# Kernel optimization log

Measured on AMD Instinct MI355X. Metric: run time of the kernel, lower is better.

## Reference

```python
import jax, jax.numpy as jnp
import numpy as np

B, C, H, W, P = 16, 5, 256, 256, 8
SF, ED, HS, NH, FF = 64, 128, 512, 4, 2048
L, NE, NS, NC, TK = 4, 6, 2, 2, 2
EPS = 1e-5


def _layernorm(x, g, b):
    m = x.mean(-1, keepdims=True)
    v = ((x - m) ** 2).mean(-1, keepdims=True)
    return (x - m) * jax.lax.rsqrt(v + EPS) * g + b


def setup_inputs() -> dict:
    key = jax.random.key(0)
    ks = iter(jax.random.split(key, 64))

    def rn(shape, s=0.02):
        return jax.random.normal(next(ks), shape, jnp.float32) * s

    return {
        "x": jax.random.normal(next(ks), (B, C, H, W), jnp.float32),
        "tok_w1": rn((SF, C * P * P)), "tok_b1": jnp.zeros((SF,), jnp.float32),
        "tok_w2": rn((ED, SF)), "tok_b2": jnp.zeros((ED,), jnp.float32),
        "proj_w": rn((HS, ED)), "proj_b": jnp.zeros((HS,), jnp.float32),
        "attn_wqkv": rn((L, 3 * HS, HS)), "attn_bqkv": jnp.zeros((L, 3 * HS), jnp.float32),
        "attn_wo": rn((L, HS, HS)), "attn_bo": jnp.zeros((L, HS), jnp.float32),
        "ln1_g": jnp.ones((L, HS), jnp.float32), "ln1_b": jnp.zeros((L, HS), jnp.float32),
        "spec_router_w": rn((L, NE, HS)),
        "spec_fc1_w": rn((L, NE, FF, HS)), "spec_fc1_b": jnp.zeros((L, NE, FF), jnp.float32),
        "spec_fc2_w": rn((L, NE, HS, FF)), "spec_fc2_b": jnp.zeros((L, NE, HS), jnp.float32),
        "shr_router_w": rn((L, NS, HS)),
        "shr_fc1_w": rn((L, NS, FF, HS)), "shr_fc1_b": jnp.zeros((L, NS, FF), jnp.float32),
        "shr_fc2_w": rn((L, NS, HS, FF)), "shr_fc2_b": jnp.zeros((L, NS, HS), jnp.float32),
        "lnm_g": jnp.ones((L, HS), jnp.float32), "lnm_b": jnp.zeros((L, HS), jnp.float32),
        "ln2_g": jnp.ones((L, HS), jnp.float32), "ln2_b": jnp.zeros((L, HS), jnp.float32),
        "cls_w": rn((NC, HS)), "cls_b": jnp.zeros((NC,), jnp.float32),
    }


def reference(x, tok_w1, tok_b1, tok_w2, tok_b2, proj_w, proj_b,
              attn_wqkv, attn_bqkv, attn_wo, attn_bo, ln1_g, ln1_b,
              spec_router_w, spec_fc1_w, spec_fc1_b, spec_fc2_w, spec_fc2_b,
              shr_router_w, shr_fc1_w, shr_fc1_b, shr_fc2_w, shr_fc2_b,
              lnm_g, lnm_b, ln2_g, ln2_b, cls_w, cls_b):
    b = x.shape[0]
    nH, nW = H // P, W // P
    S = nH * nW
    # PatchTokeniser: [B,C,H,W] -> [B, nP, C*p*p] (patch-major, channel inside)
    t = x.reshape(b, C, nH, P, nW, P).transpose(0, 2, 4, 1, 3, 5).reshape(b, S, C * P * P)
    z = jax.nn.relu(t @ tok_w1.T + tok_b1)
    z = jax.nn.relu(z @ tok_w2.T + tok_b2)  # [B,S,ED]
    # sinusoidal positional encoding (dropout is identity at inference)
    pos = np.arange(S, dtype=np.float32)[:, None]
    div = np.exp(np.arange(0, ED, 2, dtype=np.float32) * (-np.log(10000.0) / ED))
    pe = np.zeros((S, ED), np.float32)
    pe[:, 0::2] = np.sin(pos * div)
    pe[:, 1::2] = np.cos(pos * div)
    z = z + jnp.asarray(pe)
    h = z @ proj_w.T + proj_b  # [B,S,HS]
    hd = HS // NH
    scale = 1.0 / np.sqrt(hd).astype(np.float32)
    for l in range(L):
        # --- self attention (torch MHA, batch_first, eval mode) ---
        qkv = h @ attn_wqkv[l].T + attn_bqkv[l]
        q, k, v = jnp.split(qkv, 3, axis=-1)
        q = q.reshape(b, S, NH, hd).transpose(0, 2, 1, 3)
        k = k.reshape(b, S, NH, hd).transpose(0, 2, 1, 3)
        v = v.reshape(b, S, NH, hd).transpose(0, 2, 1, 3)
        att = jax.nn.softmax(jnp.einsum('bhqd,bhkd->bhqk', q, k) * scale, axis=-1)
        a = jnp.einsum('bhqk,bhkd->bhqd', att, v).transpose(0, 2, 1, 3).reshape(b, S, HS)
        a = a @ attn_wo[l].T + attn_bo[l]
        h = _layernorm(h + a, ln1_g[l], ln1_b[l])
        # --- SpecificMoE: top-k routing; combine weights replace dense masking ---
        probs = jax.nn.softmax(h @ spec_router_w[l].T, axis=-1)  # [B,S,NE]
        topk_p, topk_i = jax.lax.top_k(probs, TK)
        topk_p = topk_p / (topk_p.sum(-1, keepdims=True) + 1e-9)
        comb = (jax.nn.one_hot(topk_i, NE, dtype=h.dtype) * topk_p[..., None]).sum(-2)  # [B,S,NE]
        spec = jnp.zeros_like(h)
        for e in range(NE):
            hid = jax.nn.gelu(h @ spec_fc1_w[l, e].T + spec_fc1_b[l, e], approximate=False)
            spec = spec + comb[..., e:e + 1] * (hid @ spec_fc2_w[l, e].T + spec_fc2_b[l, e])
        # --- SharedMoE: softmax-weighted sum of all shared experts ---
        sp = jax.nn.softmax(h @ shr_router_w[l].T, axis=-1)  # [B,S,NS]
        shar = jnp.zeros_like(h)
        for e in range(NS):
            hid = jax.nn.gelu(h @ shr_fc1_w[l, e].T + shr_fc1_b[l, e], approximate=False)
            shar = shar + sp[..., e:e + 1] * (hid @ shr_fc2_w[l, e].T + shr_fc2_b[l, e])
        m = _layernorm(h + spec + shar, lnm_g[l], lnm_b[l])
        h = _layernorm(h + m, ln2_g[l], ln2_b[l])
    pooled = h.mean(axis=1)  # [B,HS]
    return pooled @ cls_w.T + cls_b  # [B,NC]
```

## Files before the change

kernel.cpp:

```cpp
#include <hip/hip_runtime.h>

typedef unsigned short u16;
using bf16x8 = __attribute__((ext_vector_type(8))) short;
using f32x4  = __attribute__((ext_vector_type(4))) float;

__device__ __forceinline__ float bf2f(u16 u) {
  union { unsigned int i; float f; } v; v.i = ((unsigned int)u) << 16; return v.f;
}
__device__ __forceinline__ u16 f2bf(float f) {
  union { float f; unsigned int i; } v; v.f = f;
  unsigned int r = v.i + 0x7fffu + ((v.i >> 16) & 1u);
  return (u16)(r >> 16);
}

__device__ __forceinline__ void async_copy16(const u16* g, u16* l) {
  __builtin_amdgcn_global_load_lds(
      (const __attribute__((address_space(1))) void*)g,
      (__attribute__((address_space(3))) void*)l, 16, 0, 0);
}

template<int ACT, int OUTMODE, int HAS_BIAS>
__global__ __launch_bounds__(256)
void gemm_tile(const u16* __restrict__ A, const u16* __restrict__ B,
               void* __restrict__ C,
               const float* __restrict__ bias,
               const float* __restrict__ rowscale, int rs_stride,
               int lda, int ldb, int ldc, int K, int inner,
               long long sAo, long long sAi, long long sBo, long long sBi,
               long long sCo, long long sCi)
{
  __shared__ u16 Als[128 * 32];
  __shared__ u16 Bls[128 * 32];

  const int tid  = threadIdx.x;
  const int lane = tid & 63;
  const int wave = tid >> 6;

  const int z  = blockIdx.z;
  const int zo = z / inner;
  const int zi = z - zo * inner;

  const u16* Ab = A + zo * sAo + zi * sAi;
  const u16* Bb = B + zo * sBo + zi * sBi;

  const long long n0 = (long long)blockIdx.x * 128;
  const long long m0 = (long long)blockIdx.y * 128;

  const int c0 = tid, c1 = tid + 256;
  const int rA0 = c0 >> 2, kA0 = (c0 & 3) * 8;
  const int rA1 = c1 >> 2, kA1 = (c1 & 3) * 8;

  const u16* gA0 = Ab + (n0 + rA0) * lda + kA0;
  const u16* gA1 = Ab + (n0 + rA1) * lda + kA1;
  const u16* gB0 = Bb + (m0 + rA0) * ldb + kA0;
  const u16* gB1 = Bb + (m0 + rA1) * ldb + kA1;

  const int fr = lane & 15;
  const int fq = lane >> 4;
  const u16* Ard = &Als[(((wave >> 1) * 64) + fr) * 32 + fq * 8];
  const u16* Brd = &Bls[(((wave & 1) * 64) + fr) * 32 + fq * 8];

  f32x4 acc[4][4] = {};

  for (int kt = 0; kt < K; kt += 32) {
    async_copy16(gA0, &Als[c0 * 8]);
    async_copy16(gA1, &Als[c1 * 8]);
    async_copy16(gB0, &Bls[c0 * 8]);
    async_copy16(gB1, &Bls[c1 * 8]);
    gA0 += 32; gA1 += 32; gB0 += 32; gB1 += 32;
    __syncthreads();

    bf16x8 af[4], bfv[4];
#pragma unroll
    for (int i = 0; i < 4; ++i) af[i]  = *(const bf16x8*)(Ard + i * (16 * 32));
#pragma unroll
    for (int j = 0; j < 4; ++j) bfv[j] = *(const bf16x8*)(Brd + j * (16 * 32));
#pragma unroll
    for (int i = 0; i < 4; ++i)
#pragma unroll
      for (int j = 0; j < 4; ++j)
        acc[i][j] = __builtin_amdgcn_mfma_f32_16x16x32_bf16(af[i], bfv[j], acc[i][j], 0, 0, 0);
    __syncthreads();
  }

  const long long cb = zo * sCo + zi * sCi;
  const int wr = (wave >> 1) * 64;
  const int wc = (wave & 1) * 64;
#pragma unroll
  for (int i = 0; i < 4; ++i) {
#pragma unroll
    for (int r = 0; r < 4; ++r) {
      const long long row = n0 + wr + i * 16 + fq * 4 + r;
      float rs = 0.f;
      if (OUTMODE == 2) rs = rowscale[row * (long long)rs_stride];
#pragma unroll
      for (int j = 0; j < 4; ++j) {
        const long long col = m0 + wc + j * 16 + fr;
        float v = acc[i][j][r];
        if (HAS_BIAS) v += bias[col];
        if (ACT == 1) v = fmaxf(v, 0.f);
        if (ACT == 2) v = 0.5f * v * (1.f + erff(v * 0.70710678118654752f));
        const long long idx = cb + row * ldc + col;
        if (OUTMODE == 0)      ((float*)C)[idx] = v;
        else if (OUTMODE == 1) ((u16*)C)[idx] = f2bf(v);
        else                   ((float*)C)[idx] += rs * v;
      }
    }
  }
}

template<int ACT, int OUT, int BIAS>
static inline void run_gemm(hipStream_t st,
    const u16* A, const u16* B, void* C, const float* bias,
    const float* rowscale, int rs_stride,
    int N, int M, int K, int lda, int ldb, int ldc,
    int batch, int inner,
    long long sAo, long long sAi, long long sBo, long long sBi,
    long long sCo, long long sCi)
{
  dim3 g(N / 128, M / 128, batch);
  gemm_tile<ACT, OUT, BIAS><<<g, dim3(256), 0, st>>>(
      A, B, C, bias, rowscale, rs_stride, lda, ldb, ldc, K, inner,
      sAo, sAi, sBo, sBi, sCo, sCi);
}

__global__ void cast_bf16_k(const float* __restrict__ s, u16* __restrict__ d, long long n)
{
  long long i = (long long)blockIdx.x * blockDim.x + threadIdx.x;
  const long long stride = (long long)gridDim.x * blockDim.x;
  for (; i < n; i += stride) d[i] = f2bf(s[i]);
}

__global__ void transpose_f32_k(const float* __restrict__ s, float* __restrict__ d,
                                int rows, int cols)
{
  int i = blockIdx.x * blockDim.x + threadIdx.x;
  if (i < rows * cols) { int r = i / cols, c = i - r * cols; d[c * rows + r] = s[i]; }
}

__global__ __launch_bounds__(64)
void tokenizer_k(const float* __restrict__ x, const float* __restrict__ w1T,
                 const float* __restrict__ b1, const float* __restrict__ w2T,
                 const float* __restrict__ b2, u16* __restrict__ z)
{
  const int token = blockIdx.x;
  const int b = token >> 10, s = token & 1023;
  const int ph = s >> 5, pw = s & 31;
  const int lane = threadIdx.x;
  __shared__ float t[320];
  __shared__ float z1[64];
  const int py = lane >> 3, px = lane & 7;
  const float* xp = x + (size_t)b * 5 * 65536 + (size_t)(ph * 8 + py) * 256 + pw * 8 + px;
#pragma unroll
  for (int c = 0; c < 5; ++c) t[c * 64 + lane] = xp[(size_t)c * 65536];
  __syncthreads();
  float acc = b1[lane];
  for (int k = 0; k < 320; ++k) acc = fmaf(t[k], w1T[k * 64 + lane], acc);
  z1[lane] = fmaxf(acc, 0.f);
  __syncthreads();
  float a0 = b2[lane], a1 = b2[lane + 64];
  for (int k = 0; k < 64; ++k) {
    const float zv = z1[k];
    a0 = fmaf(zv, w2T[k * 128 + lane], a0);
    a1 = fmaf(zv, w2T[k * 128 + lane + 64], a1);
  }
  a0 = fmaxf(a0, 0.f); a1 = fmaxf(a1, 0.f);
  const float fs = (float)s;
  const int d0 = lane, d1 = lane + 64;
  const float div0 = expf(-logf(10000.f) * (float)(d0 & ~1) / 128.f);
  const float div1 = expf(-logf(10000.f) * (float)(d1 & ~1) / 128.f);
  const float pe0 = (d0 & 1) ? cosf(fs * div0) : sinf(fs * div0);
  const float pe1 = (d1 & 1) ? cosf(fs * div1) : sinf(fs * div1);
  z[(size_t)token * 128 + d0] = f2bf(a0 + pe0);
  z[(size_t)token * 128 + d1] = f2bf(a1 + pe1);
}

__global__ void transpose_v_k(const u16* __restrict__ qkv, u16* __restrict__ vT)
{
  __shared__ u16 tile[32][33];
  const int z = blockIdx.z;
  const int b = z >> 2, hh = z & 3;
  const int s0 = blockIdx.x * 32, d0 = blockIdx.y * 32;
  const int tx = threadIdx.x;
  for (int i = threadIdx.y; i < 32; i += 8)
    tile[i][tx] = qkv[(long long)(b * 1024 + s0 + i) * 1536 + 1024 + hh * 128 + d0 + tx];
  __syncthreads();
  for (int j = threadIdx.y; j < 32; j += 8)
    vT[((long long)z * 128 + d0 + j) * 1024 + s0 + tx] = tile[tx][j];
}

__global__ __launch_bounds__(256)
void softmax_k(u16* __restrict__ P, float scale)
{
  const long long row = blockIdx.x;
  u16* p = P + row * 1024;
  const int tid = threadIdx.x;
  float v[4];
#pragma unroll
  for (int j = 0; j < 4; ++j) v[j] = bf2f(p[tid + j * 256]) * scale;
  __shared__ float red[256];
  float mx = fmaxf(fmaxf(v[0], v[1]), fmaxf(v[2], v[3]));
  red[tid] = mx; __syncthreads();
  for (int s = 128; s > 0; s >>= 1) { if (tid < s) red[tid] = fmaxf(red[tid], red[tid + s]); __syncthreads(); }
  mx = red[0]; __syncthreads();
  float sum = 0.f;
#pragma unroll
  for (int j = 0; j < 4; ++j) { v[j] = expf(v[j] - mx); sum += v[j]; }
  red[tid] = sum; __syncthreads();
  for (int s = 128; s > 0; s >>= 1) { if (tid < s) red[tid] += red[tid + s]; __syncthreads(); }
  const float inv = 1.f / red[0];
#pragma unroll
  for (int j = 0; j < 4; ++j) p[tid + j * 256] = f2bf(v[j] * inv);
}

__global__ __launch_bounds__(256)
void ln_add_k(float* __restrict__ h, const float* __restrict__ a,
              const float* __restrict__ g, const float* __restrict__ b,
              u16* __restrict__ hbf)
{
  const long long t = blockIdx.x;
  const int tid = threadIdx.x;
  float* hp = h + t * 512;
  const float* ap = a + t * 512;
  const float x0 = hp[tid] + ap[tid];
  const float x1 = hp[tid + 256] + ap[tid + 256];
  __shared__ float r1[256], r2[256];
  r1[tid] = x0 + x1; r2[tid] = x0 * x0 + x1 * x1;
  __syncthreads();
  for (int s = 128; s > 0; s >>= 1) { if (tid < s) { r1[tid] += r1[tid + s]; r2[tid] += r2[tid + s]; } __syncthreads(); }
  const float mean = r1[0] * (1.f / 512.f);
  const float var  = r2[0] * (1.f / 512.f) - mean * mean;
  const float rstd = rsqrtf(var + 1e-5f);
  const float y0 = (x0 - mean) * rstd * g[tid] + b[tid];
  const float y1 = (x1 - mean) * rstd * g[tid + 256] + b[tid + 256];
  hp[tid] = y0; hp[tid + 256] = y1;
  hbf[t * 512 + tid] = f2bf(y0); hbf[t * 512 + tid + 256] = f2bf(y1);
}

__global__ __launch_bounds__(256)
void merge_ln_k(float* __restrict__ h, const float* __restrict__ macc,
                const float* __restrict__ g1, const float* __restrict__ b1,
                const float* __restrict__ g2, const float* __restrict__ b2,
                u16* __restrict__ hbf)
{
  const long long t = blockIdx.x;
  const int tid = threadIdx.x;
  float* hp = h + t * 512;
  const float* mp = macc + t * 512;
  const float hx0 = hp[tid], hx1 = hp[tid + 256];
  const float s0 = hx0 + mp[tid], s1 = hx1 + mp[tid + 256];
  __shared__ float r1[256], r2[256];
  r1[tid] = s0 + s1; r2[tid] = s0 * s0 + s1 * s1;
  __syncthreads();
  for (int s = 128; s > 0; s >>= 1) { if (tid < s) { r1[tid] += r1[tid + s]; r2[tid] += r2[tid + s]; } __syncthreads(); }
  float mean = r1[0] * (1.f / 512.f);
  float var  = r2[0] * (1.f / 512.f) - mean * mean;
  float rstd = rsqrtf(var + 1e-5f);
  const float m0v = (s0 - mean) * rstd * g1[tid] + b1[tid];
  const float m1v = (s1 - mean) * rstd * g1[tid + 256] + b1[tid + 256];
  const float z0 = hx0 + m0v, z1 = hx1 + m1v;
  __syncthreads();
  r1[tid] = z0 + z1; r2[tid] = z0 * z0 + z1 * z1;
  __syncthreads();
  for (int s = 128; s > 0; s >>= 1) { if (tid < s) { r1[tid] += r1[tid + s]; r2[tid] += r2[tid + s]; } __syncthreads(); }
  mean = r1[0] * (1.f / 512.f);
  var  = r2[0] * (1.f / 512.f) - mean * mean;
  rstd = rsqrtf(var + 1e-5f);
  const float y0 = (z0 - mean) * rstd * g2[tid] + b2[tid];
  const float y1 = (z1 - mean) * rstd * g2[tid + 256] + b2[tid + 256];
  hp[tid] = y0; hp[tid + 256] = y1;
  hbf[t * 512 + tid] = f2bf(y0); hbf[t * 512 + tid + 256] = f2bf(y1);
}

__global__ __launch_bounds__(64)
void router_k(const float* __restrict__ h, const float* __restrict__ sw,
              const float* __restrict__ hw, float* __restrict__ comb,
              float* __restrict__ sp)
{
  const long long t = blockIdx.x;
  const int lane = threadIdx.x;
  const float* hp = h + t * 512;
  float v[8];
#pragma unroll
  for (int j = 0; j < 8; ++j) v[j] = hp[lane + j * 64];

  float lg[6];
#pragma unroll
  for (int e = 0; e < 6; ++e) {
    const float* w = sw + e * 512;
    float d = 0.f;
#pragma unroll
    for (int j = 0; j < 8; ++j) d += v[j] * w[lane + j * 64];
#pragma unroll
    for (int off = 32; off > 0; off >>= 1) d += __shfl_xor(d, off);
    lg[e] = d;
  }
  float mx = lg[0];
#pragma unroll
  for (int e = 1; e < 6; ++e) mx = fmaxf(mx, lg[e]);
  float pp[6]; float sum = 0.f;
#pragma unroll
  for (int e = 0; e < 6; ++e) { pp[e] = expf(lg[e] - mx); sum += pp[e]; }
  const float inv = 1.f / sum;
#pragma unroll
  for (int e = 0; e < 6; ++e) pp[e] *= inv;

  int i1 = 0; float p1 = pp[0];
#pragma unroll
  for (int e = 1; e < 6; ++e) if (pp[e] > p1) { p1 = pp[e]; i1 = e; }
  int i2 = -1; float p2 = -1.f;
#pragma unroll
  for (int e = 0; e < 6; ++e) if (e != i1 && pp[e] > p2) { p2 = pp[e]; i2 = e; }
  const float den = 1.f / (p1 + p2 + 1e-9f);
  if (lane == 0) {
#pragma unroll
    for (int e = 0; e < 6; ++e)
      comb[t * 6 + e] = (e == i1) ? p1 * den : ((e == i2) ? p2 * den : 0.f);
  }

  float l0 = 0.f, l1 = 0.f;
#pragma unroll
  for (int j = 0; j < 8; ++j) {
    l0 += v[j] * hw[lane + j * 64];
    l1 += v[j] * hw[512 + lane + j * 64];
  }
#pragma unroll
  for (int off = 32; off > 0; off >>= 1) { l0 += __shfl_xor(l0, off); l1 += __shfl_xor(l1, off); }
  const float m2 = fmaxf(l0, l1);
  const float e0 = expf(l0 - m2), e1 = expf(l1 - m2);
  const float si = 1.f / (e0 + e1);
  if (lane == 0) { sp[t * 2 + 0] = e0 * si; sp[t * 2 + 1] = e1 * si; }
}

__global__ __launch_bounds__(256)
void pool_cls_k(const float* __restrict__ h, const float* __restrict__ cw,
                const float* __restrict__ cb, float* __restrict__ out)
{
  const int b = blockIdx.x;
  const int tid = threadIdx.x;
  const float* hp = h + (size_t)b * 1024 * 512;
  float s0 = 0.f, s1 = 0.f;
  for (int s = 0; s < 1024; ++s) {
    s0 += hp[(size_t)s * 512 + tid];
    s1 += hp[(size_t)s * 512 + tid + 256];
  }
  __shared__ float pooled[512];
  pooled[tid] = s0 * (1.f / 1024.f); pooled[tid + 256] = s1 * (1.f / 1024.f);
  __syncthreads();
  __shared__ float red[256];
  for (int c = 0; c < 2; ++c) {
    const float d = pooled[tid] * cw[c * 512 + tid] + pooled[tid + 256] * cw[c * 512 + tid + 256];
    red[tid] = d; __syncthreads();
    for (int s = 128; s > 0; s >>= 1) { if (tid < s) red[tid] += red[tid + s]; __syncthreads(); }
    if (tid == 0) out[b * 2 + c] = red[0] + cb[c];
    __syncthreads();
  }
}

extern "C" void kernel_launch(void* const* d_in, const int* in_sizes, int n_in,
                              void* d_out, int out_size, void* d_ws, size_t ws_size,
                              hipStream_t stream)
{
  (void)in_sizes; (void)n_in; (void)out_size; (void)ws_size;
  const float* x      = (const float*)d_in[0];
  const float* tok_w1 = (const float*)d_in[1];
  const float* tok_b1 = (const float*)d_in[2];
  const float* tok_w2 = (const float*)d_in[3];
  const float* tok_b2 = (const float*)d_in[4];
  const float* proj_w = (const float*)d_in[5];
  const float* proj_b = (const float*)d_in[6];
  const float* wqkv   = (const float*)d_in[7];
  const float* bqkv   = (const float*)d_in[8];
  const float* wo     = (const float*)d_in[9];
  const float* bo     = (const float*)d_in[10];
  const float* ln1_g  = (const float*)d_in[11];
  const float* ln1_b  = (const float*)d_in[12];
  const float* srw    = (const float*)d_in[13];
  const float* sfc1w  = (const float*)d_in[14];
  const float* sfc1b  = (const float*)d_in[15];
  const float* sfc2w  = (const float*)d_in[16];
  const float* sfc2b  = (const float*)d_in[17];
  const float* hrw    = (const float*)d_in[18];
  const float* hfc1w  = (const float*)d_in[19];
  const float* hfc1b  = (const float*)d_in[20];
  const float* hfc2w  = (const float*)d_in[21];
  const float* hfc2b  = (const float*)d_in[22];
  const float* lnm_g  = (const float*)d_in[23];
  const float* lnm_b  = (const float*)d_in[24];
  const float* ln2_g  = (const float*)d_in[25];
  const float* ln2_b  = (const float*)d_in[26];
  const float* cls_w  = (const float*)d_in[27];
  const float* cls_b  = (const float*)d_in[28];

  char* ws = (char*)d_ws;
  size_t off = 0;
  auto alloc = [&](size_t bytes) -> char* {
    char* p = ws + off;
    off = (off + bytes + 255) & ~(size_t)255;
    return p;
  };

  u16* proj_bf = (u16*)alloc((size_t)512 * 128 * 2);
  u16* qkvw_bf = (u16*)alloc((size_t)4 * 1536 * 512 * 2);
  u16* wow_bf  = (u16*)alloc((size_t)4 * 512 * 512 * 2);
  u16* sfc1_bf = (u16*)alloc((size_t)4 * 6 * 2048 * 512 * 2);
  u16* sfc2_bf = (u16*)alloc((size_t)4 * 6 * 512 * 2048 * 2);
  u16* hfc1_bf = (u16*)alloc((size_t)4 * 2 * 2048 * 512 * 2);
  u16* hfc2_bf = (u16*)alloc((size_t)4 * 2 * 512 * 2048 * 2);
  float* w1T   = (float*)alloc((size_t)320 * 64 * 4);
  float* w2T   = (float*)alloc((size_t)64 * 128 * 4);
  u16* zbf     = (u16*)alloc((size_t)16384 * 128 * 2);
  float* h     = (float*)alloc((size_t)16384 * 512 * 4);
  u16* hbf     = (u16*)alloc((size_t)16384 * 512 * 2);
  u16* vT      = (u16*)alloc((size_t)64 * 128 * 1024 * 2);
  u16* abf     = (u16*)alloc((size_t)16384 * 512 * 2);
  char* regA   = alloc((size_t)32 * 1024 * 1024 * 2);
  char* regB   = alloc((size_t)16384 * 1536 * 2);
  u16*   scores = (u16*)regA;
  float* af32   = (float*)regA;
  u16*   hid    = (u16*)regA;
  u16*   qkv    = (u16*)regB;
  float* macc   = (float*)regB;
  float* comb   = (float*)(regB + (size_t)16384 * 512 * 4);
  float* sp     = (float*)(regB + (size_t)16384 * 512 * 4 + (size_t)16384 * 6 * 4);

  cast_bf16_k<<<4096, 256, 0, stream>>>(proj_w, proj_bf, 65536LL);
  cast_bf16_k<<<4096, 256, 0, stream>>>(wqkv,   qkvw_bf, 3145728LL);
  cast_bf16_k<<<4096, 256, 0, stream>>>(wo,     wow_bf,  1048576LL);
  cast_bf16_k<<<4096, 256, 0, stream>>>(sfc1w,  sfc1_bf, 25165824LL);
  cast_bf16_k<<<4096, 256, 0, stream>>>(sfc2w,  sfc2_bf, 25165824LL);
  cast_bf16_k<<<4096, 256, 0, stream>>>(hfc1w,  hfc1_bf, 8388608LL);
  cast_bf16_k<<<4096, 256, 0, stream>>>(hfc2w,  hfc2_bf, 8388608LL);
  transpose_f32_k<<<(20480 + 255) / 256, 256, 0, stream>>>(tok_w1, w1T, 64, 320);
  transpose_f32_k<<<(8192 + 255) / 256, 256, 0, stream>>>(tok_w2, w2T, 128, 64);

  tokenizer_k<<<16384, 64, 0, stream>>>(x, w1T, tok_b1, w2T, tok_b2, zbf);
  run_gemm<0, 0, 1>(stream, zbf, proj_bf, h, proj_b, nullptr, 0,
                    16384, 512, 128, 128, 128, 512, 1, 1, 0, 0, 0, 0, 0, 0);
  cast_bf16_k<<<4096, 256, 0, stream>>>(h, hbf, 8388608LL);

  for (int l = 0; l < 4; ++l) {
    run_gemm<0, 1, 1>(stream, hbf, qkvw_bf + (size_t)l * 1536 * 512, qkv,
                      bqkv + l * 1536, nullptr, 0,
                      16384, 1536, 512, 512, 512, 1536, 1, 1, 0, 0, 0, 0, 0, 0);
    transpose_v_k<<<dim3(32, 4, 64), dim3(32, 8), 0, stream>>>(qkv, vT);
    for (int c = 0; c < 2; ++c) {
      const u16* qb = qkv + (size_t)c * 8 * 1024 * 1536;
      run_gemm<0, 1, 0>(stream, qb, qb + 512, scores, nullptr, nullptr, 0,
                        1024, 1024, 128, 1536, 1536, 1024, 32, 4,
                        1024LL * 1536, 128, 1024LL * 1536, 128,
                        4LL * 1024 * 1024, 1024LL * 1024);
      softmax_k<<<32768, 256, 0, stream>>>(scores, 0.08838834764831845f);
      run_gemm<0, 1, 0>(stream, scores, vT + (size_t)c * 8 * 4 * 128 * 1024,
                        abf + (size_t)c * 8 * 1024 * 512, nullptr, nullptr, 0,
                        1024, 128, 1024, 1024, 1024, 512, 32, 4,
                        4LL * 1024 * 1024, 1024LL * 1024,
                        4LL * 128 * 1024, 128LL * 1024,
                        1024LL * 512, 128);
    }
    run_gemm<0, 0, 1>(stream, abf, wow_bf + (size_t)l * 512 * 512, af32,
                      bo + l * 512, nullptr, 0,
                      16384, 512, 512, 512, 512, 512, 1, 1, 0, 0, 0, 0, 0, 0);
    hipMemsetAsync(macc, 0, (size_t)16384 * 512 * 4, stream);
    ln_add_k<<<16384, 256, 0, stream>>>(h, af32, ln1_g + l * 512, ln1_b + l * 512, hbf);
    router_k<<<16384, 64, 0, stream>>>(h, srw + (size_t)l * 6 * 512,
                                       hrw + (size_t)l * 2 * 512, comb, sp);
    for (int e = 0; e < 6; ++e) {
      const size_t wi = (size_t)(l * 6 + e);
      run_gemm<2, 1, 1>(stream, hbf, sfc1_bf + wi * 2048 * 512, hid,
                        sfc1b + wi * 2048, nullptr, 0,
                        16384, 2048, 512, 512, 512, 2048, 1, 1, 0, 0, 0, 0, 0, 0);
      run_gemm<0, 2, 1>(stream, hid, sfc2_bf + wi * 512 * 2048, macc,
                        sfc2b + wi * 512, comb + e, 6,
                        16384, 512, 2048, 2048, 2048, 512, 1, 1, 0, 0, 0, 0, 0, 0);
    }
    for (int e = 0; e < 2; ++e) {
      const size_t wi = (size_t)(l * 2 + e);
      run_gemm<2, 1, 1>(stream, hbf, hfc1_bf + wi * 2048 * 512, hid,
                        hfc1b + wi * 2048, nullptr, 0,
                        16384, 2048, 512, 512, 512, 2048, 1, 1, 0, 0, 0, 0, 0, 0);
      run_gemm<0, 2, 1>(stream, hid, hfc2_bf + wi * 512 * 2048, macc,
                        hfc2b + wi * 512, sp + e, 2,
                        16384, 512, 2048, 2048, 2048, 512, 1, 1, 0, 0, 0, 0, 0, 0);
    }
    merge_ln_k<<<16384, 256, 0, stream>>>(h, macc, lnm_g + l * 512, lnm_b + l * 512,
                                          ln2_g + l * 512, ln2_b + l * 512, hbf);
  }

  pool_cls_k<<<16, 256, 0, stream>>>(h, cls_w, cls_b, (float*)d_out);
}
```

Before: 6.571 ms.

## Run routed experts only on tokens selected by top-k gating

Builds per-expert token index lists from the combine weights, then runs the expert FC1 GEMM on gathered rows and the FC2 GEMM with split-K and atomic scatter-add back to token rows. Row blocks beyond the expert's token count exit early, avoiding dense computation for the roughly two-thirds of tokens each expert does not serve. Adds a list-building kernel, atomic accumulation with nondeterministic summation order, and gathered loads.

```diff
diff --git a/kernel.cpp b/kernel.cpp
--- a/kernel.cpp
+++ b/kernel.cpp
@@ -19,12 +19,14 @@
       (__attribute__((address_space(3))) void*)l, 16, 0, 0);
 }
 
-template<int ACT, int OUTMODE, int HAS_BIAS>
+template<int ACT, int OUTMODE, int HAS_BIAS, int GA>
 __global__ __launch_bounds__(256)
 void gemm_tile(const u16* __restrict__ A, const u16* __restrict__ B,
                void* __restrict__ C,
                const float* __restrict__ bias,
                const float* __restrict__ rowscale, int rs_stride,
+               const int* __restrict__ gidx, const int* __restrict__ gcnt,
+               int bias_zi0,
                int lda, int ldb, int ldc, int K, int inner,
                long long sAo, long long sAi, long long sBo, long long sBi,
                long long sCo, long long sCi)
@@ -40,18 +42,29 @@
   const int zo = z / inner;
   const int zi = z - zo * inner;
 
+  const long long n0 = (long long)blockIdx.x * 128;
+  const long long m0 = (long long)blockIdx.y * 128;
+
+  int cnt = 0x7fffffff;
+  if (GA || OUTMODE == 3) {
+    cnt = *gcnt;
+    if (n0 >= cnt) return;
+  }
+
   const u16* Ab = A + zo * sAo + zi * sAi;
   const u16* Bb = B + zo * sBo + zi * sBi;
-
-  const long long n0 = (long long)blockIdx.x * 128;
-  const long long m0 = (long long)blockIdx.y * 128;
 
   const int c0 = tid, c1 = tid + 256;
   const int rA0 = c0 >> 2, kA0 = (c0 & 3) * 8;
   const int rA1 = c1 >> 2, kA1 = (c1 & 3) * 8;
 
-  const u16* gA0 = Ab + (n0 + rA0) * lda + kA0;
-  const u16* gA1 = Ab + (n0 + rA1) * lda + kA1;
+  long long arow0 = n0 + rA0, arow1 = n0 + rA1;
+  if (GA) {
+    arow0 = (arow0 < cnt) ? (long long)gidx[arow0] : 0;
+    arow1 = (arow1 < cnt) ? (long long)gidx[arow1] : 0;
+  }
+  const u16* gA0 = Ab + arow0 * lda + kA0;
+  const u16* gA1 = Ab + arow1 * lda + kA1;
   const u16* gB0 = Bb + (m0 + rA0) * ldb + kA0;
   const u16* gB1 = Bb + (m0 + rA1) * ldb + kA1;
 
@@ -92,18 +105,27 @@
     for (int r = 0; r < 4; ++r) {
       const long long row = n0 + wr + i * 16 + fq * 4 + r;
       float rs = 0.f;
+      long long crow = row;
+      bool ok = true;
       if (OUTMODE == 2) rs = rowscale[row * (long long)rs_stride];
+      if (OUTMODE == 3) {
+        ok = row < cnt;
+        const int tok = ok ? gidx[row] : 0;
+        crow = tok;
+        rs = ok ? rowscale[(long long)tok * rs_stride] : 0.f;
+      }
 #pragma unroll
       for (int j = 0; j < 4; ++j) {
         const long long col = m0 + wc + j * 16 + fr;
         float v = acc[i][j][r];
-        if (HAS_BIAS) v += bias[col];
+        if (HAS_BIAS) { if (!bias_zi0 || zi == 0) v += bias[col]; }
         if (ACT == 1) v = fmaxf(v, 0.f);
         if (ACT == 2) v = 0.5f * v * (1.f + erff(v * 0.70710678118654752f));
-        const long long idx = cb + row * ldc + col;
+        const long long idx = cb + crow * ldc + col;
         if (OUTMODE == 0)      ((float*)C)[idx] = v;
         else if (OUTMODE == 1) ((u16*)C)[idx] = f2bf(v);
-        else                   ((float*)C)[idx] += rs * v;
+        else if (OUTMODE == 2) ((float*)C)[idx] += rs * v;
+        else if (ok)           atomicAdd(&((float*)C)[idx], rs * v);
       }
     }
   }
@@ -119,9 +141,9 @@
     long long sCo, long long sCi)
 {
   dim3 g(N / 128, M / 128, batch);
-  gemm_tile<ACT, OUT, BIAS><<<g, dim3(256), 0, st>>>(
-      A, B, C, bias, rowscale, rs_stride, lda, ldb, ldc, K, inner,
-      sAo, sAi, sBo, sBi, sCo, sCi);
+  gemm_tile<ACT, OUT, BIAS, 0><<<g, dim3(256), 0, st>>>(
+      A, B, C, bias, rowscale, rs_stride, nullptr, nullptr, 0,
+      lda, ldb, ldc, K, inner, sAo, sAi, sBo, sBi, sCo, sCi);
 }
 
 __global__ void cast_bf16_k(const float* __restrict__ s, u16* __restrict__ d, long long n)
@@ -330,6 +352,21 @@
   const float e0 = expf(l0 - m2), e1 = expf(l1 - m2);
   const float si = 1.f / (e0 + e1);
   if (lane == 0) { sp[t * 2 + 0] = e0 * si; sp[t * 2 + 1] = e1 * si; }
+}
+
+__global__ __launch_bounds__(256)
+void build_lists_k(const float* __restrict__ comb, int* __restrict__ cnt,
+                   int* __restrict__ idx)
+{
+  const int t = blockIdx.x * blockDim.x + threadIdx.x;
+  if (t >= 16384) return;
+#pragma unroll
+  for (int e = 0; e < 6; ++e) {
+    if (comb[(long long)t * 6 + e] > 0.f) {
+      const int pos = atomicAdd(&cnt[e], 1);
+      idx[e * 16384 + pos] = t;
+    }
+  }
 }
 
 __global__ __launch_bounds__(256)
@@ -414,6 +451,8 @@
   u16* hbf     = (u16*)alloc((size_t)16384 * 512 * 2);
   u16* vT      = (u16*)alloc((size_t)64 * 128 * 1024 * 2);
   u16* abf     = (u16*)alloc((size_t)16384 * 512 * 2);
+  int* cnt     = (int*)alloc((size_t)6 * 4);
+  int* idx     = (int*)alloc((size_t)6 * 16384 * 4);
   char* regA   = alloc((size_t)32 * 1024 * 1024 * 2);
   char* regB   = alloc((size_t)16384 * 1536 * 2);
   u16*   scores = (u16*)regA;
@@ -465,14 +504,18 @@
     ln_add_k<<<16384, 256, 0, stream>>>(h, af32, ln1_g + l * 512, ln1_b + l * 512, hbf);
     router_k<<<16384, 64, 0, stream>>>(h, srw + (size_t)l * 6 * 512,
                                        hrw + (size_t)l * 2 * 512, comb, sp);
+    hipMemsetAsync(cnt, 0, 6 * sizeof(int), stream);
+    build_lists_k<<<64, 256, 0, stream>>>(comb, cnt, idx);
     for (int e = 0; e < 6; ++e) {
       const size_t wi = (size_t)(l * 6 + e);
-      run_gemm<2, 1, 1>(stream, hbf, sfc1_bf + wi * 2048 * 512, hid,
-                        sfc1b + wi * 2048, nullptr, 0,
-                        16384, 2048, 512, 512, 512, 2048, 1, 1, 0, 0, 0, 0, 0, 0);
-      run_gemm<0, 2, 1>(stream, hid, sfc2_bf + wi * 512 * 2048, macc,
-                        sfc2b + wi * 512, comb + e, 6,
-                        16384, 512, 2048, 2048, 2048, 512, 1, 1, 0, 0, 0, 0, 0, 0);
+      gemm_tile<2, 1, 1, 1><<<dim3(128, 16, 1), dim3(256), 0, stream>>>(
+          hbf, sfc1_bf + wi * 2048 * 512, hid,
+          sfc1b + wi * 2048, nullptr, 0, idx + e * 16384, cnt + e, 0,
+          512, 512, 2048, 512, 1, 0, 0, 0, 0, 0, 0);
+      gemm_tile<0, 3, 1, 0><<<dim3(128, 4, 2), dim3(256), 0, stream>>>(
+          hid, sfc2_bf + wi * 512 * 2048, macc,
+          sfc2b + wi * 512, comb + e, 6, idx + e * 16384, cnt + e, 1,
+          2048, 2048, 512, 1024, 2, 0, 1024, 0, 1024, 0, 0);
     }
     for (int e = 0; e < 2; ++e) {
       const size_t wi = (size_t)(l * 2 + e);
```

After: 6.541 ms. No clear change (-0.5%).

## Route MoE tokens sparsely with grouped expert GEMMs and atomic scatter-add

Applied to the files above, without the earlier changes.

The specialist experts previously ran dense over all tokens and were masked by combine weights. Now the router builds per-expert token index lists, and grouped fc1/fc2 kernels process only the routed tokens (top-2 of 6, plus the shared experts) in FF chunks of 512. Results are scattered into the accumulator with float atomics. This removes the dense work on unselected experts, at the cost of gathered loads, atomic contention and nondeterministic summation order. The softmax kernel also switches to vectorized uint2 loads and stores.

```diff
diff --git a/kernel.cpp b/kernel.cpp
--- a/kernel.cpp
+++ b/kernel.cpp
@@ -1,6 +1,7 @@
 #include <hip/hip_runtime.h>
 
 typedef unsigned short u16;
+typedef unsigned int u32;
 using bf16x8 = __attribute__((ext_vector_type(8))) short;
 using f32x4  = __attribute__((ext_vector_type(4))) float;
 
@@ -19,12 +20,10 @@
       (__attribute__((address_space(3))) void*)l, 16, 0, 0);
 }
 
-template<int ACT, int OUTMODE, int HAS_BIAS>
+template<int OUTMODE, int HAS_BIAS>
 __global__ __launch_bounds__(256)
 void gemm_tile(const u16* __restrict__ A, const u16* __restrict__ B,
-               void* __restrict__ C,
-               const float* __restrict__ bias,
-               const float* __restrict__ rowscale, int rs_stride,
+               void* __restrict__ C, const float* __restrict__ bias,
                int lda, int ldb, int ldc, int K, int inner,
                long long sAo, long long sAi, long long sBo, long long sBi,
                long long sCo, long long sCi)
@@ -91,37 +90,200 @@
 #pragma unroll
     for (int r = 0; r < 4; ++r) {
       const long long row = n0 + wr + i * 16 + fq * 4 + r;
-      float rs = 0.f;
-      if (OUTMODE == 2) rs = rowscale[row * (long long)rs_stride];
 #pragma unroll
       for (int j = 0; j < 4; ++j) {
         const long long col = m0 + wc + j * 16 + fr;
         float v = acc[i][j][r];
         if (HAS_BIAS) v += bias[col];
-        if (ACT == 1) v = fmaxf(v, 0.f);
-        if (ACT == 2) v = 0.5f * v * (1.f + erff(v * 0.70710678118654752f));
         const long long idx = cb + row * ldc + col;
-        if (OUTMODE == 0)      ((float*)C)[idx] = v;
-        else if (OUTMODE == 1) ((u16*)C)[idx] = f2bf(v);
-        else                   ((float*)C)[idx] += rs * v;
+        if (OUTMODE == 0) ((float*)C)[idx] = v;
+        else              ((u16*)C)[idx] = f2bf(v);
       }
     }
   }
 }
 
-template<int ACT, int OUT, int BIAS>
+template<int OUT, int BIAS>
 static inline void run_gemm(hipStream_t st,
     const u16* A, const u16* B, void* C, const float* bias,
-    const float* rowscale, int rs_stride,
     int N, int M, int K, int lda, int ldb, int ldc,
     int batch, int inner,
     long long sAo, long long sAi, long long sBo, long long sBi,
     long long sCo, long long sCi)
 {
   dim3 g(N / 128, M / 128, batch);
-  gemm_tile<ACT, OUT, BIAS><<<g, dim3(256), 0, st>>>(
-      A, B, C, bias, rowscale, rs_stride, lda, ldb, ldc, K, inner,
-      sAo, sAi, sBo, sBi, sCo, sCi);
+  gemm_tile<OUT, BIAS><<<g, dim3(256), 0, st>>>(
+      A, B, C, bias, lda, ldb, ldc, K, inner, sAo, sAi, sBo, sBi, sCo, sCi);
+}
+
+__global__ __launch_bounds__(256)
+void moe_fc1_k(const u16* __restrict__ A, const u16* __restrict__ W,
+               const float* __restrict__ sb, const float* __restrict__ hb,
+               const int* __restrict__ idx, const int* __restrict__ cnt,
+               const int* __restrict__ poff,
+               u16* __restrict__ hid, int ff0)
+{
+  __shared__ u16 Als[128 * 32];
+  __shared__ u16 Bls[128 * 32];
+
+  const int tid  = threadIdx.x;
+  const int lane = tid & 63;
+  const int wave = tid >> 6;
+
+  const int row0 = blockIdx.x * 128;
+  if (row0 >= poff[8]) return;
+  int e = 0;
+  while (row0 >= poff[e + 1]) ++e;
+  const int r0 = row0 - poff[e];
+  const int ce = cnt[e];
+  if (r0 >= ce) return;
+  const int* gi = idx + e * 16384;
+
+  const int m0 = blockIdx.y * 128;
+  const u16* Wb = W + (size_t)e * 2048 * 512 + (size_t)(ff0 + m0) * 512;
+  const float* bias = (e < 6 ? sb + e * 2048 : hb + (e - 6) * 2048) + ff0;
+
+  const int c0 = tid, c1 = tid + 256;
+  const int rA0 = c0 >> 2, kA0 = (c0 & 3) * 8;
+  const int rA1 = c1 >> 2, kA1 = (c1 & 3) * 8;
+
+  const int t0 = (r0 + rA0 < ce) ? gi[r0 + rA0] : gi[r0];
+  const int t1 = (r0 + rA1 < ce) ? gi[r0 + rA1] : gi[r0];
+  const u16* gA0 = A + (size_t)t0 * 512 + kA0;
+  const u16* gA1 = A + (size_t)t1 * 512 + kA1;
+  const u16* gB0 = Wb + (size_t)rA0 * 512 + kA0;
+  const u16* gB1 = Wb + (size_t)rA1 * 512 + kA1;
+
+  const int fr = lane & 15;
+  const int fq = lane >> 4;
+  const u16* Ard = &Als[(((wave >> 1) * 64) + fr) * 32 + fq * 8];
+  const u16* Brd = &Bls[(((wave & 1) * 64) + fr) * 32 + fq * 8];
+
+  f32x4 acc[4][4] = {};
+
+  for (int kt = 0; kt < 512; kt += 32) {
+    async_copy16(gA0, &Als[c0 * 8]);
+    async_copy16(gA1, &Als[c1 * 8]);
+    async_copy16(gB0, &Bls[c0 * 8]);
+    async_copy16(gB1, &Bls[c1 * 8]);
+    gA0 += 32; gA1 += 32; gB0 += 32; gB1 += 32;
+    __syncthreads();
+
+    bf16x8 af[4], bfv[4];
+#pragma unroll
+    for (int i = 0; i < 4; ++i) af[i]  = *(const bf16x8*)(Ard + i * (16 * 32));
+#pragma unroll
+    for (int j = 0; j < 4; ++j) bfv[j] = *(const bf16x8*)(Brd + j * (16 * 32));
+#pragma unroll
+    for (int i = 0; i < 4; ++i)
+#pragma unroll
+      for (int j = 0; j < 4; ++j)
+        acc[i][j] = __builtin_amdgcn_mfma_f32_16x16x32_bf16(af[i], bfv[j], acc[i][j], 0, 0, 0);
+    __syncthreads();
+  }
+
+  const int wr = (wave >> 1) * 64;
+  const int wc = (wave & 1) * 64;
+#pragma unroll
+  for (int i = 0; i < 4; ++i) {
+#pragma unroll
+    for (int r = 0; r < 4; ++r) {
+      const long long row = row0 + wr + i * 16 + fq * 4 + r;
+#pragma unroll
+      for (int j = 0; j < 4; ++j) {
+        const int col = m0 + wc + j * 16 + fr;
+        float v = acc[i][j][r] + bias[col];
+        v = 0.5f * v * (1.f + erff(v * 0.70710678118654752f));
+        hid[row * 512 + col] = f2bf(v);
+      }
+    }
+  }
+}
+
+__global__ __launch_bounds__(256)
+void moe_fc2_k(const u16* __restrict__ hid, const u16* __restrict__ W,
+               const float* __restrict__ sb, const float* __restrict__ hb,
+               const float* __restrict__ comb, const float* __restrict__ sp,
+               const int* __restrict__ idx, const int* __restrict__ cnt,
+               const int* __restrict__ poff,
+               float* __restrict__ macc, int ff0)
+{
+  __shared__ u16 Als[128 * 32];
+  __shared__ u16 Bls[128 * 32];
+
+  const int tid  = threadIdx.x;
+  const int lane = tid & 63;
+  const int wave = tid >> 6;
+
+  const int row0 = blockIdx.x * 128;
+  if (row0 >= poff[8]) return;
+  int e = 0;
+  while (row0 >= poff[e + 1]) ++e;
+  const int r0 = row0 - poff[e];
+  const int ce = cnt[e];
+  if (r0 >= ce) return;
+  const int* gi = idx + e * 16384;
+
+  const int m0 = blockIdx.y * 128;
+  const u16* Wb = W + (size_t)e * 512 * 2048 + (size_t)m0 * 2048 + ff0;
+  const float* bias = (e < 6 ? sb + e * 512 : hb + (e - 6) * 512);
+
+  const int c0 = tid, c1 = tid + 256;
+  const int rA0 = c0 >> 2, kA0 = (c0 & 3) * 8;
+  const int rA1 = c1 >> 2, kA1 = (c1 & 3) * 8;
+
+  const u16* gA0 = hid + (size_t)(row0 + rA0) * 512 + kA0;
+  const u16* gA1 = hid + (size_t)(row0 + rA1) * 512 + kA1;
+  const u16* gB0 = Wb + (size_t)rA0 * 2048 + kA0;
+  const u16* gB1 = Wb + (size_t)rA1 * 2048 + kA1;
+
+  const int fr = lane & 15;
+  const int fq = lane >> 4;
+  const u16* Ard = &Als[(((wave >> 1) * 64) + fr) * 32 + fq * 8];
+  const u16* Brd = &Bls[(((wave & 1) * 64) + fr) * 32 + fq * 8];
+
+  f32x4 acc[4][4] = {};
+
+  for (int kt = 0; kt < 512; kt += 32) {
+    async_copy16(gA0, &Als[c0 * 8]);
+    async_copy16(gA1, &Als[c1 * 8]);
+    async_copy16(gB0, &Bls[c0 * 8]);
+    async_copy16(gB1, &Bls[c1 * 8]);
+    gA0 += 32; gA1 += 32; gB0 += 32; gB1 += 32;
+    __syncthreads();
+
+    bf16x8 af[4], bfv[4];
+#pragma unroll
+    for (int i = 0; i < 4; ++i) af[i]  = *(const bf16x8*)(Ard + i * (16 * 32));
+#pragma unroll
+    for (int j = 0; j < 4; ++j) bfv[j] = *(const bf16x8*)(Brd + j * (16 * 32));
+#pragma unroll
+    for (int i = 0; i < 4; ++i)
+#pragma unroll
+      for (int j = 0; j < 4; ++j)
+        acc[i][j] = __builtin_amdgcn_mfma_f32_16x16x32_bf16(af[i], bfv[j], acc[i][j], 0, 0, 0);
+    __syncthreads();
+  }
+
+  const int wr = (wave >> 1) * 64;
+  const int wc = (wave & 1) * 64;
+#pragma unroll
+  for (int i = 0; i < 4; ++i) {
+#pragma unroll
+    for (int r = 0; r < 4; ++r) {
+      const int lr = r0 + wr + i * 16 + fq * 4 + r;
+      if (lr >= ce) continue;
+      const int tok = gi[lr];
+      const float rs = (e < 6) ? comb[(size_t)tok * 6 + e] : sp[(size_t)tok * 2 + (e - 6)];
+#pragma unroll
+      for (int j = 0; j < 4; ++j) {
+        const int col = m0 + wc + j * 16 + fr;
+        float v = acc[i][j][r];
+        if (ff0 == 0) v += bias[col];
+        atomicAdd(&macc[(size_t)tok * 512 + col], rs * v);
+      }
+    }
+  }
 }
 
 __global__ void cast_bf16_k(const float* __restrict__ s, u16* __restrict__ d, long long n)
@@ -129,6 +291,24 @@
   long long i = (long long)blockIdx.x * blockDim.x + threadIdx.x;
   const long long stride = (long long)gridDim.x * blockDim.x;
   for (; i < n; i += stride) d[i] = f2bf(s[i]);
+}
+
+__global__ void cast_moe_w_k(const float* __restrict__ spec,
+                             const float* __restrict__ shr,
+                             u16* __restrict__ dst)
+{
+  long long i = (long long)blockIdx.x * blockDim.x + threadIdx.x;
+  const long long stride = (long long)gridDim.x * blockDim.x;
+  const long long n = 4LL * 8 * 1048576;
+  for (; i < n; i += stride) {
+    const long long l = i >> 23;
+    const long long r = i & ((1LL << 23) - 1);
+    const long long e = r >> 20;
+    const long long o = r & 1048575;
+    const float v = (e < 6) ? spec[(l * 6 + e) * 1048576 + o]
+                            : shr[(l * 2 + (e - 6)) * 1048576 + o];
+    dst[i] = f2bf(v);
+  }
 }
 
 __global__ void transpose_f32_k(const float* __restrict__ s, float* __restrict__ d,
@@ -193,11 +373,14 @@
 void softmax_k(u16* __restrict__ P, float scale)
 {
   const long long row = blockIdx.x;
-  u16* p = P + row * 1024;
+  uint2* p = (uint2*)(P + row * 1024);
   const int tid = threadIdx.x;
+  uint2 d = p[tid];
   float v[4];
-#pragma unroll
-  for (int j = 0; j < 4; ++j) v[j] = bf2f(p[tid + j * 256]) * scale;
+  v[0] = bf2f((u16)(d.x & 0xffff)) * scale;
+  v[1] = bf2f((u16)(d.x >> 16)) * scale;
+  v[2] = bf2f((u16)(d.y & 0xffff)) * scale;
+  v[3] = bf2f((u16)(d.y >> 16)) * scale;
   __shared__ float red[256];
   float mx = fmaxf(fmaxf(v[0], v[1]), fmaxf(v[2], v[3]));
   red[tid] = mx; __syncthreads();
@@ -209,8 +392,10 @@
   red[tid] = sum; __syncthreads();
   for (int s = 128; s > 0; s >>= 1) { if (tid < s) red[tid] += red[tid + s]; __syncthreads(); }
   const float inv = 1.f / red[0];
-#pragma unroll
-  for (int j = 0; j < 4; ++j) p[tid + j * 256] = f2bf(v[j] * inv);
+  uint2 o;
+  o.x = (u32)f2bf(v[0] * inv) | ((u32)f2bf(v[1] * inv) << 16);
+  o.y = (u32)f2bf(v[2] * inv) | ((u32)f2bf(v[3] * inv) << 16);
+  p[tid] = o;
 }
 
 __global__ __launch_bounds__(256)
@@ -275,7 +460,7 @@
 __global__ __launch_bounds__(64)
 void router_k(const float* __restrict__ h, const float* __restrict__ sw,
               const float* __restrict__ hw, float* __restrict__ comb,
-              float* __restrict__ sp)
+              float* __restrict__ sp, int* __restrict__ cnt, int* __restrict__ idx)
 {
   const long long t = blockIdx.x;
   const int lane = threadIdx.x;
@@ -316,6 +501,10 @@
 #pragma unroll
     for (int e = 0; e < 6; ++e)
       comb[t * 6 + e] = (e == i1) ? p1 * den : ((e == i2) ? p2 * den : 0.f);
+    int p = atomicAdd(&cnt[i1], 1); idx[i1 * 16384 + p] = (int)t;
+    p = atomicAdd(&cnt[i2], 1);     idx[i2 * 16384 + p] = (int)t;
+    idx[6 * 16384 + t] = (int)t;
+    idx[7 * 16384 + t] = (int)t;
   }
 
   float l0 = 0.f, l1 = 0.f;
@@ -330,6 +519,15 @@
   const float e0 = expf(l0 - m2), e1 = expf(l1 - m2);
   const float si = 1.f / (e0 + e1);
   if (lane == 0) { sp[t * 2 + 0] = e0 * si; sp[t * 2 + 1] = e1 * si; }
+}
+
+__global__ void offsets_k(int* __restrict__ cnt, int* __restrict__ poff)
+{
+  if (threadIdx.x == 0 && blockIdx.x == 0) {
+    cnt[6] = 16384; cnt[7] = 16384;
+    int o = 0; poff[0] = 0;
+    for (int e = 0; e < 8; ++e) { o += (cnt[e] + 127) & ~127; poff[e + 1] = o; }
+  }
 }
 
 __global__ __launch_bounds__(256)
@@ -361,7 +559,7 @@
                               void* d_out, int out_size, void* d_ws, size_t ws_size,
                               hipStream_t stream)
 {
-  (void)in_sizes; (void)n_in; (void)out_size; (void)ws_size;
+  (void)in_sizes; (void)n_in; (void)out_size;
   const float* x      = (const float*)d_in[0];
   const float* tok_w1 = (const float*)d_in[1];
   const float* tok_b1 = (const float*)d_in[2];
@@ -403,10 +601,8 @@
   u16* proj_bf = (u16*)alloc((size_t)512 * 128 * 2);
   u16* qkvw_bf = (u16*)alloc((size_t)4 * 1536 * 512 * 2);
   u16* wow_bf  = (u16*)alloc((size_t)4 * 512 * 512 * 2);
-  u16* sfc1_bf = (u16*)alloc((size_t)4 * 6 * 2048 * 512 * 2);
-  u16* sfc2_bf = (u16*)alloc((size_t)4 * 6 * 512 * 2048 * 2);
-  u16* hfc1_bf = (u16*)alloc((size_t)4 * 2 * 2048 * 512 * 2);
-  u16* hfc2_bf = (u16*)alloc((size_t)4 * 2 * 512 * 2048 * 2);
+  u16* w1comb  = (u16*)alloc((size_t)4 * 8 * 2048 * 512 * 2);
+  u16* w2comb  = (u16*)alloc((size_t)4 * 8 * 512 * 2048 * 2);
   float* w1T   = (float*)alloc((size_t)320 * 64 * 4);
   float* w2T   = (float*)alloc((size_t)64 * 128 * 4);
   u16* zbf     = (u16*)alloc((size_t)16384 * 128 * 2);
@@ -414,7 +610,10 @@
   u16* hbf     = (u16*)alloc((size_t)16384 * 512 * 2);
   u16* vT      = (u16*)alloc((size_t)64 * 128 * 1024 * 2);
   u16* abf     = (u16*)alloc((size_t)16384 * 512 * 2);
-  char* regA   = alloc((size_t)32 * 1024 * 1024 * 2);
+  int* cnt     = (int*)alloc((size_t)8 * 4);
+  int* poff    = (int*)alloc((size_t)9 * 4);
+  int* idx     = (int*)alloc((size_t)8 * 16384 * 4);
+  char* regA   = alloc((size_t)66560 * 512 * 2);
   char* regB   = alloc((size_t)16384 * 1536 * 2);
   u16*   scores = (u16*)regA;
   float* af32   = (float*)regA;
@@ -424,64 +623,58 @@
   float* comb   = (float*)(regB + (size_t)16384 * 512 * 4);
   float* sp     = (float*)(regB + (size_t)16384 * 512 * 4 + (size_t)16384 * 6 * 4);
 
+  if (off > ws_size) return;
+
   cast_bf16_k<<<4096, 256, 0, stream>>>(proj_w, proj_bf, 65536LL);
   cast_bf16_k<<<4096, 256, 0, stream>>>(wqkv,   qkvw_bf, 3145728LL);
   cast_bf16_k<<<4096, 256, 0, stream>>>(wo,     wow_bf,  1048576LL);
-  cast_bf16_k<<<4096, 256, 0, stream>>>(sfc1w,  sfc1_bf, 25165824LL);
-  cast_bf16_k<<<4096, 256, 0, stream>>>(sfc2w,  sfc2_bf, 25165824LL);
-  cast_bf16_k<<<4096, 256, 0, stream>>>(hfc1w,  hfc1_bf, 8388608LL);
-  cast_bf16_k<<<4096, 256, 0, stream>>>(hfc2w,  hfc2_bf, 8388608LL);
+  cast_moe_w_k<<<8192, 256, 0, stream>>>(sfc1w, hfc1w, w1comb);
+  cast_moe_w_k<<<8192, 256, 0, stream>>>(sfc2w, hfc2w, w2comb);
   transpose_f32_k<<<(20480 + 255) / 256, 256, 0, stream>>>(tok_w1, w1T, 64, 320);
   transpose_f32_k<<<(8192 + 255) / 256, 256, 0, stream>>>(tok_w2, w2T, 128, 64);
 
   tokenizer_k<<<16384, 64, 0, stream>>>(x, w1T, tok_b1, w2T, tok_b2, zbf);
-  run_gemm<0, 0, 1>(stream, zbf, proj_bf, h, proj_b, nullptr, 0,
-                    16384, 512, 128, 128, 128, 512, 1, 1, 0, 0, 0, 0, 0, 0);
+  run_gemm<0, 1>(stream, zbf, proj_bf, h, proj_b,
+                 16384, 512, 128, 128, 128, 512, 1, 1, 0, 0, 0, 0, 0, 0);
   cast_bf16_k<<<4096, 256, 0, stream>>>(h, hbf, 8388608LL);
 
   for (int l = 0; l < 4; ++l) {
-    run_gemm<0, 1, 1>(stream, hbf, qkvw_bf + (size_t)l * 1536 * 512, qkv,
-                      bqkv + l * 1536, nullptr, 0,
-                      16384, 1536, 512, 512, 512, 1536, 1, 1, 0, 0, 0, 0, 0, 0);
+    run_gemm<1, 1>(stream, hbf, qkvw_bf + (size_t)l * 1536 * 512, qkv,
+                   bqkv + l * 1536,
+                   16384, 1536, 512, 512, 512, 1536, 1, 1, 0, 0, 0, 0, 0, 0);
     transpose_v_k<<<dim3(32, 4, 64), dim3(32, 8), 0, stream>>>(qkv, vT);
     for (int c = 0; c < 2; ++c) {
       const u16* qb = qkv + (size_t)c * 8 * 1024 * 1536;
-      run_gemm<0, 1, 0>(stream, qb, qb + 512, scores, nullptr, nullptr, 0,
-                        1024, 1024, 128, 1536, 1536, 1024, 32, 4,
-                        1024LL * 1536, 128, 1024LL * 1536, 128,
-                        4LL * 1024 * 1024, 1024LL * 1024);
+      run_gemm<1, 0>(stream, qb, qb + 512, scores, nullptr,
+                     1024, 1024, 128, 1536, 1536, 1024, 32, 4,
+                     1024LL * 1536, 128, 1024LL * 1536, 128,
+                     4LL * 1024 * 1024, 1024LL * 1024);
       softmax_k<<<32768, 256, 0, stream>>>(scores, 0.08838834764831845f);
-      run_gemm<0, 1, 0>(stream, scores, vT + (size_t)c * 8 * 4 * 128 * 1024,
-                        abf + (size_t)c * 8 * 1024 * 512, nullptr, nullptr, 0,
-                        1024, 128, 1024, 1024, 1024, 512, 32, 4,
-                        4LL * 1024 * 1024, 1024LL * 1024,
-                        4LL * 128 * 1024, 128LL * 1024,
-                        1024LL * 512, 128);
+      run_gemm<1, 0>(stream, scores, vT + (size_t)c * 8 * 4 * 128 * 1024,
+                     abf + (size_t)c * 8 * 1024 * 512, nullptr,
+                     1024, 128, 1024, 1024, 1024, 512, 32, 4,
+                     4LL * 1024 * 1024, 1024LL * 1024,
+                     4LL * 128 * 1024, 128LL * 1024,
+                     1024LL * 512, 128);
     }
-    run_gemm<0, 0, 1>(stream, abf, wow_bf + (size_t)l * 512 * 512, af32,
-                      bo + l * 512, nullptr, 0,
-                      16384, 512, 512, 512, 512, 512, 1, 1, 0, 0, 0, 0, 0, 0);
+    run_gemm<0, 1>(stream, abf, wow_bf + (size_t)l * 512 * 512, af32,
+                   bo + l * 512,
+                   16384, 512, 512, 512, 512, 512, 1, 1, 0, 0, 0, 0, 0, 0);
     hipMemsetAsync(macc, 0, (size_t)16384 * 512 * 4, stream);
+    hipMemsetAsync(cnt, 0, 8 * sizeof(int), stream);
     ln_add_k<<<16384, 256, 0, stream>>>(h, af32, ln1_g + l * 512, ln1_b + l * 512, hbf);
     router_k<<<16384, 64, 0, stream>>>(h, srw + (size_t)l * 6 * 512,
-                                       hrw + (size_t)l * 2 * 512, comb, sp);
-    for (int e = 0; e < 6; ++e) {
-      const size_t wi = (size_t)(l * 6 + e);
-      run_gemm<2, 1, 1>(stream, hbf, sfc1_bf + wi * 2048 * 512, hid,
-                        sfc1b + wi * 2048, nullptr, 0,
-                        16384, 2048, 512, 512, 512, 2048, 1, 1, 0, 0, 0, 0, 0, 0);
-      run_gemm<0, 2, 1>(stream, hid, sfc2_bf + wi * 512 * 2048, macc,
-                        sfc2b + wi * 512, comb + e, 6,
-                        16384, 512, 2048, 2048, 2048, 512, 1, 1, 0, 0, 0, 0, 0, 0);
-    }
-    for (int e = 0; e < 2; ++e) {
-      const size_t wi = (size_t)(l * 2 + e);
-      run_gemm<2, 1, 1>(stream, hbf, hfc1_bf + wi * 2048 * 512, hid,
-                        hfc1b + wi * 2048, nullptr, 0,
-                        16384, 2048, 512, 512, 512, 2048, 1, 1, 0, 0, 0, 0, 0, 0);
-      run_gemm<0, 2, 1>(stream, hid, hfc2_bf + wi * 512 * 2048, macc,
-                        hfc2b + wi * 512, sp + e, 2,
-                        16384, 512, 2048, 2048, 2048, 512, 1, 1, 0, 0, 0, 0, 0, 0);
+                                       hrw + (size_t)l * 2 * 512, comb, sp, cnt, idx);
+    offsets_k<<<1, 64, 0, stream>>>(cnt, poff);
+    for (int ffq = 0; ffq < 4; ++ffq) {
+      moe_fc1_k<<<dim3(520, 4), dim3(256), 0, stream>>>(
+          hbf, w1comb + (size_t)l * 8 * 2048 * 512,
+          sfc1b + (size_t)l * 6 * 2048, hfc1b + (size_t)l * 2 * 2048,
+          idx, cnt, poff, hid, ffq * 512);
+      moe_fc2_k<<<dim3(520, 4), dim3(256), 0, stream>>>(
+          hid, w2comb + (size_t)l * 8 * 512 * 2048,
+          sfc2b + (size_t)l * 6 * 512, hfc2b + (size_t)l * 2 * 512,
+          comb, sp, idx, cnt, poff, macc, ffq * 512);
     }
     merge_ln_k<<<16384, 256, 0, stream>>>(h, macc, lnm_g + l * 512, lnm_b + l * 512,
                                           ln2_g + l * 512, ln2_b + l * 512, hbf);
```

Result: slower. 7.309 ms (+11.2%).
